# Optimization experiments

Measured on AMD Instinct MI355X. Metric: run time of the kernel, lower is better.

The kernel has to match this reference:

```python
import jax, jax.numpy as jnp
import numpy as np

B, T, D = 8, 4096, 1024
E, H = 8, 32  # n_experts, hidden_dim


def setup_inputs() -> dict:
    key = jax.random.key(0)
    ks = jax.random.split(key, 8)
    s = 1.0 / np.sqrt(D)
    sh = 1.0 / np.sqrt(H)
    return {
        "x": jax.random.normal(ks[0], (B, T, D), dtype=jnp.float32),
        "Wr": jax.random.uniform(ks[1], (D, E), jnp.float32, -s, s),
        "br": jax.random.uniform(ks[2], (E,), jnp.float32, -s, s),
        "W1": jax.random.uniform(ks[3], (E, D, 2 * H), jnp.float32, -s, s),
        "b1": jax.random.uniform(ks[4], (E, 2 * H), jnp.float32, -s, s),
        "W2": jax.random.uniform(ks[5], (E, H, D), jnp.float32, -sh, sh),
        "b2": jax.random.uniform(ks[6], (E, D), jnp.float32, -sh, sh),
    }


def reference(x, Wr, br, W1, b1, W2, b2):
    # Router: softmax gate over experts, [B,T,E]
    probs = jax.nn.softmax(x @ Wr + br, axis=-1)
    # All experts densely: h [B,E,T,2H]
    h = jnp.einsum('btd,edh->beth', x, W1) + b1[:, None, :]
    xp, gate = jnp.split(h, 2, axis=-1)  # chunk(2, dim=-1): first half value, second half gate
    act = xp * jax.nn.silu(gate)         # SwiGLU; dropout = identity (eval)
    out_e = jnp.einsum('beth,ehd->betd', act, W2) + b2[:, None, :]
    # Softmax-weighted sum over experts
    out = jnp.einsum('betd,bte->btd', out_e, probs)
    return out
```

## Files before the change

kernel.cpp:

```cpp
#include <hip/hip_runtime.h>

typedef float f32x4 __attribute__((ext_vector_type(4)));
typedef short bf16x8 __attribute__((ext_vector_type(8)));

#define B1S_KBSZ 67584
#define W2S_OFF  1081344
#define ACT_OFF  1736704

__device__ __forceinline__ unsigned short f2bf(float f) {
  unsigned int u = __float_as_uint(f);
  return (unsigned short)((u + 0x7FFFu + ((u >> 16) & 1u)) >> 16);
}
__device__ __forceinline__ unsigned int pack2(float a, float b) {
  return (unsigned int)f2bf(a) | ((unsigned int)f2bf(b) << 16);
}
__device__ __forceinline__ unsigned int cvtpk(float a, float b) {
  unsigned int r;
  asm("v_cvt_pk_bf16_f32 %0, %1, %2" : "=v"(r) : "v"(a), "v"(b));
  return r;
}

__global__ __launch_bounds__(256) void prep_all(const float* __restrict__ W1,
                                                const float* __restrict__ Wr,
                                                const float* __restrict__ W2,
                                                const float* __restrict__ b2,
                                                unsigned char* __restrict__ B1s,
                                                unsigned char* __restrict__ W2s) {
  if (blockIdx.x < 264) {
    int t = blockIdx.x * 256 + threadIdx.x;
    int c   = t & 7;
    int col = (t >> 3) % 528;
    int kb  = (t >> 3) / 528;
    int e   = col >> 6;
    int hh  = col & 63;
    float v[8];
    #pragma unroll
    for (int jj = 0; jj < 8; ++jj) {
      int k = kb * 64 + c * 8 + jj;
      float f;
      if (col < 512)      f = W1[(e * 1024 + k) * 64 + hh];
      else if (col < 520) f = Wr[k * 8 + (col - 512)];
      else                f = 0.0f;
      v[jj] = f;
    }
    *(uint4*)(B1s + kb * B1S_KBSZ + col * 128 + ((c ^ (col & 7)) * 16)) =
        make_uint4(pack2(v[0], v[1]), pack2(v[2], v[3]), pack2(v[4], v[5]), pack2(v[6], v[7]));
  } else {
    int t = (blockIdx.x - 264) * 256 + threadIdx.x;
    int cj  = t % 40;
    int col = t / 40;
    float v[8];
    #pragma unroll
    for (int jj = 0; jj < 8; ++jj) {
      int k = cj * 8 + jj;
      float f;
      if (k < 256)      f = W2[k * 1024 + col];
      else if (k < 264) f = b2[(k - 256) * 1024 + col];
      else              f = 0.0f;
      v[jj] = f;
    }
    int dstc = (cj & ~7) | ((cj & 7) ^ (col & 7));
    *(uint4*)(W2s + col * 640 + dstc * 16) =
        make_uint4(pack2(v[0], v[1]), pack2(v[2], v[3]), pack2(v[4], v[5]), pack2(v[6], v[7]));
  }
}

__global__ __launch_bounds__(256) void cvt_x(const float* __restrict__ x,
                                             unsigned char* __restrict__ xbf) {
  int t = blockIdx.x * 256 + threadIdx.x;
  int row = t >> 7, c = t & 127;
  const float* s = x + (size_t)row * 1024 + c * 8;
  f32x4 a = *(const f32x4*)s;
  f32x4 b = *(const f32x4*)(s + 4);
  uint4 u;
  u.x = cvtpk(a.x, a.y); u.y = cvtpk(a.z, a.w);
  u.z = cvtpk(b.x, b.y); u.w = cvtpk(b.z, b.w);
  *(uint4*)(xbf + (size_t)row * 2048 + (((c & ~7) | ((c & 7) ^ (row & 7))) << 4)) = u;
}

__global__ __launch_bounds__(256, 3) void moe_gemm1(
    const unsigned char* __restrict__ xbf, const float* __restrict__ br,
    const float* __restrict__ b1, const unsigned char* __restrict__ B1s,
    unsigned char* __restrict__ ACT) {
  __shared__ __align__(16) unsigned char smem[30720];

  const int tid  = threadIdx.x;
  const int lane = tid & 63;
  const int w    = tid >> 6;
  const int f15  = lane & 15;
  const int fhi  = lane >> 4;
  const int k7   = f15 & 7;

  const int wid  = ((blockIdx.x & 7) << 7) + (blockIdx.x >> 3);
  const int mt   = wid >> 1;
  const int half = wid & 1;
  const int m0   = mt << 6;
  const int e    = half * 4 + w;

  f32x4 acc[4][4];
  f32x4 accR[4];
  #pragma unroll
  for (int a = 0; a < 4; ++a) {
    #pragma unroll
    for (int b = 0; b < 4; ++b) acc[a][b] = f32x4{0.f, 0.f, 0.f, 0.f};
    accR[a] = f32x4{0.f, 0.f, 0.f, 0.f};
  }

  const unsigned char* aB  = xbf + (size_t)(m0 + f15) * 2048;
  const unsigned char* bp  = B1s + (size_t)(e * 64 + f15) * 128;
  const unsigned char* brt = B1s + (size_t)(512 + f15) * 128;
  const int ch0 = ((fhi)     ^ k7) << 4;
  const int ch1 = ((4 + fhi) ^ k7) << 4;

  #pragma unroll
  for (int ks = 0; ks < 16; ++ks) {
    const size_t kso = (size_t)ks * B1S_KBSZ;
    const bool doR = ((ks >> 2) == w);
    bf16x8 a0[4], a1[4];
    #pragma unroll
    for (int mf = 0; mf < 4; ++mf) {
      const unsigned char* s_ = aB + mf * 32768 + ks * 128;
      a0[mf] = *(const bf16x8*)(s_ + ch0);
      a1[mf] = *(const bf16x8*)(s_ + ch1);
    }
    #pragma unroll
    for (int i = 0; i < 4; ++i) {
      const unsigned char* s_ = bp + kso + i * 2048;
      bf16x8 b0  = *(const bf16x8*)(s_ + ch0);
      bf16x8 b1v = *(const bf16x8*)(s_ + ch1);
      #pragma unroll
      for (int mf = 0; mf < 4; ++mf)
        acc[mf][i] = __builtin_amdgcn_mfma_f32_16x16x32_bf16(a0[mf], b0, acc[mf][i], 0, 0, 0);
      #pragma unroll
      for (int mf = 0; mf < 4; ++mf)
        acc[mf][i] = __builtin_amdgcn_mfma_f32_16x16x32_bf16(a1[mf], b1v, acc[mf][i], 0, 0, 0);
    }
    if (doR) {
      bf16x8 r0 = *(const bf16x8*)(brt + kso + ch0);
      bf16x8 r1 = *(const bf16x8*)(brt + kso + ch1);
      #pragma unroll
      for (int mf = 0; mf < 4; ++mf)
        accR[mf] = __builtin_amdgcn_mfma_f32_16x16x32_bf16(a0[mf], r0, accR[mf], 0, 0, 0);
      #pragma unroll
      for (int mf = 0; mf < 4; ++mf)
        accR[mf] = __builtin_amdgcn_mfma_f32_16x16x32_bf16(a1[mf], r1, accR[mf], 0, 0, 0);
    }
    if ((ks & 3) == 3) __syncthreads();
  }

  unsigned short* hb = (unsigned short*)smem;
  float* logitP = (float*)(smem + 17408);
  float* logit  = (float*)(smem + 25600);
  float* pb     = (float*)(smem + 27648);

  if (f15 < 8) {
    #pragma unroll
    for (int mf = 0; mf < 4; ++mf)
      #pragma unroll
      for (int r = 0; r < 4; ++r)
        logitP[(w * 64 + mf * 16 + fhi * 4 + r) * 8 + f15] = accR[mf][r];
  }
  __syncthreads();
  {
    int row = tid >> 2, ep = tid & 3;
    #pragma unroll
    for (int j = 0; j < 2; ++j) {
      int ee = ep * 2 + j;
      float s = logitP[row * 8 + ee] + logitP[(64 + row) * 8 + ee] +
                logitP[(128 + row) * 8 + ee] + logitP[(192 + row) * 8 + ee];
      logit[row * 8 + ee] = s + br[ee];
    }
  }
  __syncthreads();
  if (tid < 64) {
    int row = tid;
    const float* lg = logit + row * 8;
    float l0 = lg[0], l1 = lg[1], l2 = lg[2], l3 = lg[3];
    float l4 = lg[4], l5 = lg[5], l6 = lg[6], l7 = lg[7];
    float mx = fmaxf(fmaxf(fmaxf(l0, l1), fmaxf(l2, l3)),
                     fmaxf(fmaxf(l4, l5), fmaxf(l6, l7)));
    float e0 = __expf(l0 - mx), e1 = __expf(l1 - mx), e2 = __expf(l2 - mx), e3 = __expf(l3 - mx);
    float e4 = __expf(l4 - mx), e5 = __expf(l5 - mx), e6 = __expf(l6 - mx), e7 = __expf(l7 - mx);
    float rinv = 1.f / (e0 + e1 + e2 + e3 + e4 + e5 + e6 + e7);
    float p_[8] = {e0 * rinv, e1 * rinv, e2 * rinv, e3 * rinv,
                   e4 * rinv, e5 * rinv, e6 * rinv, e7 * rinv};
    #pragma unroll
    for (int j = 0; j < 8; ++j) {
      pb[row * 8 + j] = p_[j];
      hb[row * 136 + 128 + j] = f2bf(p_[j]);
    }
  }
  __syncthreads();
  {
    const float b1x0 = b1[e * 64 + f15],      b1x1 = b1[e * 64 + 16 + f15];
    const float b1g0 = b1[e * 64 + 32 + f15], b1g1 = b1[e * 64 + 48 + f15];
    #pragma unroll
    for (int mf = 0; mf < 4; ++mf) {
      #pragma unroll
      for (int r = 0; r < 4; ++r) {
        int row = mf * 16 + fhi * 4 + r;
        float pe = pb[row * 8 + e];
        #pragma unroll
        for (int ci = 0; ci < 2; ++ci) {
          float xv = acc[mf][ci][r]     + (ci ? b1x1 : b1x0);
          float gv = acc[mf][ci + 2][r] + (ci ? b1g1 : b1g0);
          float av = pe * xv * gv / (1.f + __expf(-gv));
          hb[row * 136 + w * 32 + ci * 16 + f15] = f2bf(av);
        }
      }
    }
  }
  __syncthreads();
  {
    const int row = tid >> 2, q = tid & 3, key = row & 7;
    unsigned char* arow = ACT + (size_t)(m0 + row) * 640;
    const unsigned char* hrow = (const unsigned char*)(hb + row * 136);
    #pragma unroll
    for (int j = 0; j < 4; ++j) {
      int c = q + j * 4;
      int g = half * 16 + c;
      uint4 v = *(const uint4*)(hrow + c * 16);
      *(uint4*)(arow + (g >> 3) * 128 + (((g & 7) ^ key) << 4)) = v;
    }
    if (half == 0) {
      #pragma unroll
      for (int j = 0; j < 2; ++j) {
        int c = q + j * 4;
        int g = 32 + c;
        uint4 v = make_uint4(0, 0, 0, 0);
        if (c == 0) v = *(const uint4*)(hrow + 256);
        *(uint4*)(arow + (g >> 3) * 128 + (((g & 7) ^ key) << 4)) = v;
      }
    }
  }
}

__global__ __launch_bounds__(256, 3) void moe_gemm2(
    const unsigned char* __restrict__ ACT, const unsigned char* __restrict__ W2s,
    float* __restrict__ out) {
  __shared__ __align__(16) unsigned char smem[32768];
  const int tid  = threadIdx.x;
  const int lane = tid & 63;
  const int w    = tid >> 6;
  const int mg   = w >> 1, ng = w & 1;
  const int f15  = lane & 15, fhi = lane >> 4;
  const int k7   = f15 & 7;

  const int wid = ((blockIdx.x & 7) << 8) + (blockIdx.x >> 3);
  const int m0  = (wid >> 3) * 128;
  const int n0  = (wid & 7) * 128;

  f32x4 acc[4][4];
  #pragma unroll
  for (int a = 0; a < 4; ++a)
    #pragma unroll
    for (int b = 0; b < 4; ++b) acc[a][b] = f32x4{0.f, 0.f, 0.f, 0.f};

  const unsigned char* aB = ACT + (size_t)(m0 + mg * 64 + f15) * 640;
  const unsigned char* bB = W2s + (size_t)(n0 + ng * 64 + f15) * 640;
  const int ch0 = ((fhi)     ^ k7) << 4;
  const int ch1 = ((4 + fhi) ^ k7) << 4;

  #pragma unroll
  for (int kb = 0; kb < 5; ++kb) {
    bf16x8 a0[4], a1[4];
    #pragma unroll
    for (int mf = 0; mf < 4; ++mf) {
      const unsigned char* s_ = aB + mf * 10240 + kb * 128;
      a0[mf] = *(const bf16x8*)(s_ + ch0);
      a1[mf] = *(const bf16x8*)(s_ + ch1);
    }
    #pragma unroll
    for (int nf = 0; nf < 4; ++nf) {
      const unsigned char* s_ = bB + nf * 10240 + kb * 128;
      bf16x8 b0 = *(const bf16x8*)(s_ + ch0);
      bf16x8 b1v = *(const bf16x8*)(s_ + ch1);
      #pragma unroll
      for (int mf = 0; mf < 4; ++mf)
        acc[mf][nf] = __builtin_amdgcn_mfma_f32_16x16x32_bf16(a0[mf], b0, acc[mf][nf], 0, 0, 0);
      #pragma unroll
      for (int mf = 0; mf < 4; ++mf)
        acc[mf][nf] = __builtin_amdgcn_mfma_f32_16x16x32_bf16(a1[mf], b1v, acc[mf][nf], 0, 0, 0);
    }
  }

  float* slab = (float*)smem;
  #pragma unroll 1
  for (int q = 0; q < 2; ++q) {
    if (mg == q) {
      #pragma unroll
      for (int mf = 0; mf < 4; ++mf)
        #pragma unroll
        for (int nf = 0; nf < 4; ++nf)
          #pragma unroll
          for (int r = 0; r < 4; ++r) {
            int rl  = mf * 16 + fhi * 4 + r;
            int col = ng * 64 + nf * 16 + f15;
            slab[rl * 128 + (col ^ (((rl >> 2) & 7) << 2))] = acc[mf][nf][r];
          }
    }
    __syncthreads();
    #pragma unroll
    for (int j = 0; j < 8; ++j) {
      int rl = (tid >> 5) + j * 8;
      int c4 = tid & 31;
      f32x4 v = *(const f32x4*)(smem + rl * 512 + ((c4 ^ ((rl >> 2) & 7)) << 4));
      *(f32x4*)(out + (size_t)(m0 + q * 64 + rl) * 1024 + n0 + c4 * 4) = v;
    }
    __syncthreads();
  }
}

extern "C" void kernel_launch(void* const* d_in, const int* in_sizes, int n_in,
                              void* d_out, int out_size, void* d_ws, size_t ws_size,
                              hipStream_t stream) {
  const float* x  = (const float*)d_in[0];
  const float* Wr = (const float*)d_in[1];
  const float* br = (const float*)d_in[2];
  const float* W1 = (const float*)d_in[3];
  const float* b1 = (const float*)d_in[4];
  const float* W2 = (const float*)d_in[5];
  const float* b2 = (const float*)d_in[6];
  float* out = (float*)d_out;
  unsigned char* ws  = (unsigned char*)d_ws;
  unsigned char* B1s = ws;
  unsigned char* W2s = ws + W2S_OFF;
  unsigned char* ACT = ws + ACT_OFF;
  unsigned char* xbf = (unsigned char*)d_out;

  hipLaunchKernelGGL(prep_all, dim3(424), dim3(256), 0, stream, W1, Wr, W2, b2, B1s, W2s);
  hipLaunchKernelGGL(cvt_x, dim3(16384), dim3(256), 0, stream, x, xbf);
  hipLaunchKernelGGL(moe_gemm1, dim3(1024), dim3(256), 0, stream, xbf, br, b1, B1s, ACT);
  hipLaunchKernelGGL(moe_gemm2, dim3(2048), dim3(256), 0, stream, ACT, W2s, out);
}
```

Before: 165.6 us.

## Prefetch B tiles in gemm1 and drop x swizzle in conversion

The conversion kernel now handles 16 floats per thread and writes bf16 rows contiguously with no XOR swizzle, and gemm1 reads A with matching unswizzled offsets. Gemm1 register-double-buffers the B1 weight fragments, loading the next k-step's tiles while the current MFMAs run, and hoists the router-weight loads ahead of the MFMA chain. Occupancy is lowered from 3 to 2 blocks per SM to make room for the extra registers, which risks less latency hiding across waves. Unswizzled A reads from global memory may also change the access pattern.

```diff
diff --git a/kernel.cpp b/kernel.cpp
--- a/kernel.cpp
+++ b/kernel.cpp
@@ -68,17 +68,23 @@
 __global__ __launch_bounds__(256) void cvt_x(const float* __restrict__ x,
                                              unsigned char* __restrict__ xbf) {
   int t = blockIdx.x * 256 + threadIdx.x;
-  int row = t >> 7, c = t & 127;
-  const float* s = x + (size_t)row * 1024 + c * 8;
+  int row = t >> 6, c2 = t & 63;
+  const float* s = x + (size_t)row * 1024 + c2 * 16;
   f32x4 a = *(const f32x4*)s;
   f32x4 b = *(const f32x4*)(s + 4);
-  uint4 u;
-  u.x = cvtpk(a.x, a.y); u.y = cvtpk(a.z, a.w);
-  u.z = cvtpk(b.x, b.y); u.w = cvtpk(b.z, b.w);
-  *(uint4*)(xbf + (size_t)row * 2048 + (((c & ~7) | ((c & 7) ^ (row & 7))) << 4)) = u;
-}
-
-__global__ __launch_bounds__(256, 3) void moe_gemm1(
+  f32x4 c = *(const f32x4*)(s + 8);
+  f32x4 d = *(const f32x4*)(s + 12);
+  uint4 u0, u1;
+  u0.x = cvtpk(a.x, a.y); u0.y = cvtpk(a.z, a.w);
+  u0.z = cvtpk(b.x, b.y); u0.w = cvtpk(b.z, b.w);
+  u1.x = cvtpk(c.x, c.y); u1.y = cvtpk(c.z, c.w);
+  u1.z = cvtpk(d.x, d.y); u1.w = cvtpk(d.z, d.w);
+  unsigned char* dst = xbf + (size_t)row * 2048 + c2 * 32;
+  *(uint4*)dst = u0;
+  *(uint4*)(dst + 16) = u1;
+}
+
+__global__ __launch_bounds__(256, 2) void moe_gemm1(
     const unsigned char* __restrict__ xbf, const float* __restrict__ br,
     const float* __restrict__ b1, const unsigned char* __restrict__ B1s,
     unsigned char* __restrict__ ACT) {
@@ -107,43 +113,67 @@
   }
 
   const unsigned char* aB  = xbf + (size_t)(m0 + f15) * 2048;
+  const int chA0 = fhi << 4;
+  const int chA1 = (4 + fhi) << 4;
   const unsigned char* bp  = B1s + (size_t)(e * 64 + f15) * 128;
   const unsigned char* brt = B1s + (size_t)(512 + f15) * 128;
   const int ch0 = ((fhi)     ^ k7) << 4;
   const int ch1 = ((4 + fhi) ^ k7) << 4;
 
+  bf16x8 b0c[4], b1c[4];
+  #pragma unroll
+  for (int i = 0; i < 4; ++i) {
+    b0c[i] = *(const bf16x8*)(bp + i * 2048 + ch0);
+    b1c[i] = *(const bf16x8*)(bp + i * 2048 + ch1);
+  }
+
   #pragma unroll
   for (int ks = 0; ks < 16; ++ks) {
     const size_t kso = (size_t)ks * B1S_KBSZ;
     const bool doR = ((ks >> 2) == w);
+
+    bf16x8 b0n[4], b1n[4];
+    if (ks < 15) {
+      const size_t ksn = kso + B1S_KBSZ;
+      #pragma unroll
+      for (int i = 0; i < 4; ++i) {
+        b0n[i] = *(const bf16x8*)(bp + ksn + i * 2048 + ch0);
+        b1n[i] = *(const bf16x8*)(bp + ksn + i * 2048 + ch1);
+      }
+    }
     bf16x8 a0[4], a1[4];
     #pragma unroll
     for (int mf = 0; mf < 4; ++mf) {
       const unsigned char* s_ = aB + mf * 32768 + ks * 128;
-      a0[mf] = *(const bf16x8*)(s_ + ch0);
-      a1[mf] = *(const bf16x8*)(s_ + ch1);
-    }
+      a0[mf] = *(const bf16x8*)(s_ + chA0);
+      a1[mf] = *(const bf16x8*)(s_ + chA1);
+    }
+    bf16x8 r0, r1;
+    if (doR) {
+      r0 = *(const bf16x8*)(brt + kso + ch0);
+      r1 = *(const bf16x8*)(brt + kso + ch1);
+    }
+
     #pragma unroll
     for (int i = 0; i < 4; ++i) {
-      const unsigned char* s_ = bp + kso + i * 2048;
-      bf16x8 b0  = *(const bf16x8*)(s_ + ch0);
-      bf16x8 b1v = *(const bf16x8*)(s_ + ch1);
-      #pragma unroll
-      for (int mf = 0; mf < 4; ++mf)
-        acc[mf][i] = __builtin_amdgcn_mfma_f32_16x16x32_bf16(a0[mf], b0, acc[mf][i], 0, 0, 0);
-      #pragma unroll
-      for (int mf = 0; mf < 4; ++mf)
-        acc[mf][i] = __builtin_amdgcn_mfma_f32_16x16x32_bf16(a1[mf], b1v, acc[mf][i], 0, 0, 0);
+      #pragma unroll
+      for (int mf = 0; mf < 4; ++mf)
+        acc[mf][i] = __builtin_amdgcn_mfma_f32_16x16x32_bf16(a0[mf], b0c[i], acc[mf][i], 0, 0, 0);
+      #pragma unroll
+      for (int mf = 0; mf < 4; ++mf)
+        acc[mf][i] = __builtin_amdgcn_mfma_f32_16x16x32_bf16(a1[mf], b1c[i], acc[mf][i], 0, 0, 0);
     }
     if (doR) {
-      bf16x8 r0 = *(const bf16x8*)(brt + kso + ch0);
-      bf16x8 r1 = *(const bf16x8*)(brt + kso + ch1);
       #pragma unroll
       for (int mf = 0; mf < 4; ++mf)
         accR[mf] = __builtin_amdgcn_mfma_f32_16x16x32_bf16(a0[mf], r0, accR[mf], 0, 0, 0);
       #pragma unroll
       for (int mf = 0; mf < 4; ++mf)
         accR[mf] = __builtin_amdgcn_mfma_f32_16x16x32_bf16(a1[mf], r1, accR[mf], 0, 0, 0);
+    }
+    if (ks < 15) {
+      #pragma unroll
+      for (int i = 0; i < 4; ++i) { b0c[i] = b0n[i]; b1c[i] = b1n[i]; }
     }
     if ((ks & 3) == 3) __syncthreads();
   }
@@ -329,7 +359,7 @@
   unsigned char* xbf = (unsigned char*)d_out;
 
   hipLaunchKernelGGL(prep_all, dim3(424), dim3(256), 0, stream, W1, Wr, W2, b2, B1s, W2s);
-  hipLaunchKernelGGL(cvt_x, dim3(16384), dim3(256), 0, stream, x, xbf);
+  hipLaunchKernelGGL(cvt_x, dim3(8192), dim3(256), 0, stream, x, xbf);
   hipLaunchKernelGGL(moe_gemm1, dim3(1024), dim3(256), 0, stream, xbf, br, b1, B1s, ACT);
   hipLaunchKernelGGL(moe_gemm2, dim3(2048), dim3(256), 0, stream, ACT, W2s, out);
 }
```

Result: slower. 174.7 us (+5.5%).
